# Kernel optimization log

Hardware: AMD Instinct MI355X
Metric: run time of the kernel (lower is better)

## Reference

```python
import jax, jax.numpy as jnp
import numpy as np

N_NODES = 10000
N_EDGES = 640000
IN_DIM = 128
NUM_HEADS = 8
OUT_DIM = 16  # per-head dim; NUM_HEADS*OUT_DIM == IN_DIM


def setup_inputs() -> dict:
    key = jax.random.key(0)
    ks = jax.random.split(key, 12)
    h = jax.random.normal(ks[0], (N_NODES, IN_DIM), dtype=jnp.float32)
    e = jax.random.normal(ks[1], (N_EDGES, IN_DIM), dtype=jnp.float32)
    src = jax.random.randint(ks[2], (N_EDGES,), 0, N_NODES, dtype=jnp.int32)
    dst = jax.random.randint(ks[3], (N_EDGES,), 0, N_NODES, dtype=jnp.int32)
    HD = NUM_HEADS * OUT_DIM
    scale = 0.05
    Wq = jax.random.normal(ks[4], (HD, IN_DIM), dtype=jnp.float32) * scale
    bq = jax.random.normal(ks[5], (HD,), dtype=jnp.float32) * scale
    Wk = jax.random.normal(ks[6], (HD, IN_DIM), dtype=jnp.float32) * scale
    bk = jax.random.normal(ks[7], (HD,), dtype=jnp.float32) * scale
    We = jax.random.normal(ks[8], (HD, IN_DIM), dtype=jnp.float32) * scale
    be = jax.random.normal(ks[9], (HD,), dtype=jnp.float32) * scale
    Wv = jax.random.normal(ks[10], (HD, IN_DIM), dtype=jnp.float32) * scale
    bv = jax.random.normal(ks[11], (HD,), dtype=jnp.float32) * scale
    return {"h": h, "e": e, "src": src, "dst": dst,
            "Wq": Wq, "bq": bq, "Wk": Wk, "bk": bk,
            "We": We, "be": be, "Wv": Wv, "bv": bv}


def reference(h, e, src, dst, Wq, bq, Wk, bk, We, be, Wv, bv):
    N = h.shape[0]
    H, D = NUM_HEADS, OUT_DIM
    # Linear projections (torch Linear: x @ W.T + b), reshape to [*, H, D]
    Q_h = (h @ Wq.T + bq).reshape(N, H, D)
    K_h = (h @ Wk.T + bk).reshape(N, H, D)
    V_h = (h @ Wv.T + bv).reshape(N, H, D)
    E_e = (e @ We.T + be).reshape(-1, H, D)
    # per-edge score: (K[src] * Q[dst]) / sqrt(D) * E  -> exp(clamp(sum(-1)))
    score = K_h[src] * Q_h[dst] / jnp.sqrt(jnp.float32(D)) * E_e  # [E, H, D]
    score_soft = jnp.exp(jnp.clip(score.sum(-1, keepdims=True), -5.0, 5.0))  # [E, H, 1]
    # scatter-sum aggregation to destination nodes
    wV = jax.ops.segment_sum(V_h[src] * score_soft, dst, num_segments=N)  # [N, H, D]
    z = jax.ops.segment_sum(score_soft, dst, num_segments=N)  # [N, H, 1]
    h_out = wV / (z + 1e-6)
    # dropout p=0.0 (eval): identity
    return h_out
```

## Files before the change

### kernel.cpp

```cpp
#include <hip/hip_runtime.h>
#include <hip/hip_bf16.h>

#define N_NODES 10000
#define N_EDGES 640000
#define HD 128
#define NH 8
#define TPAD 136

typedef __attribute__((ext_vector_type(4))) float floatx4;
typedef __attribute__((ext_vector_type(8))) __bf16 bf16x8;

__device__ __forceinline__ float b2f(unsigned short u) {
    union { unsigned int i; float f; } x;
    x.i = ((unsigned int)u) << 16;
    return x.f;
}
__device__ __forceinline__ unsigned short f2b(float f) {
    union { float f; unsigned int i; } x; x.f = f;
    unsigned int r = x.i + 0x7FFF + ((x.i >> 16) & 1);
    return (unsigned short)(r >> 16);
}

template<bool F32>
__device__ __forceinline__ float ld1(const void* p, size_t i) {
    if (F32) return ((const float*)p)[i];
    return b2f(((const unsigned short*)p)[i]);
}
template<bool F32>
__device__ __forceinline__ void ld8(const void* p, size_t i, float* out) {
    if (F32) {
        floatx4 a = *(const floatx4*)((const float*)p + i);
        floatx4 b = *(const floatx4*)((const float*)p + i + 4);
        out[0]=a[0]; out[1]=a[1]; out[2]=a[2]; out[3]=a[3];
        out[4]=b[0]; out[5]=b[1]; out[6]=b[2]; out[7]=b[3];
    } else {
        uint4 u = *(const uint4*)((const unsigned short*)p + i);
        const unsigned short* s = (const unsigned short*)&u;
        #pragma unroll
        for (int j = 0; j < 8; ++j) out[j] = b2f(s[j]);
    }
}
template<bool F32>
__device__ __forceinline__ uint4 ld8b(const void* p, size_t i) {
    if (F32) {
        float f[8]; ld8<true>(p, i, f);
        union { unsigned short s[8]; uint4 u; } r;
        #pragma unroll
        for (int j = 0; j < 8; ++j) r.s[j] = f2b(f[j]);
        return r.u;
    }
    return *(const uint4*)((const unsigned short*)p + i);
}

__global__ void k_sniff(const unsigned short* __restrict__ h,
                        int* __restrict__ wcnt, int* __restrict__ flag) {
    int t = threadIdx.x;
    int w = 0;
    #pragma unroll
    for (int j = 0; j < 16; ++j) {
        unsigned short u = h[t * 16 + j];
        int ex = (u >> 7) & 0xFF;
        if (ex >= 0x8F) ++w;
    }
    atomicAdd(wcnt, w);
    __threadfence();
    __syncthreads();
    if (t == 0) {
        int c = atomicAdd(wcnt, 0);
        *flag = (c > 64) ? 1 : 0;
    }
}

template<bool F32>
__device__ __forceinline__ void qkv_body(
    float (*hs)[HD],
    const void* __restrict__ h,
    const void* __restrict__ Wq, const void* __restrict__ bq,
    const void* __restrict__ Wk, const void* __restrict__ bk,
    const void* __restrict__ Wv, const void* __restrict__ bv,
    float* __restrict__ Qs, float* __restrict__ Kg, float* __restrict__ Vg)
{
    const int n0 = blockIdx.x * 8;
    const int d = threadIdx.x;
    #pragma unroll
    for (int r = 0; r < 8; ++r)
        hs[r][d] = ld1<F32>(h, (size_t)(n0 + r) * HD + d);
    __syncthreads();

    float aq[8], ak[8], av[8];
    #pragma unroll
    for (int i = 0; i < 8; ++i) { aq[i] = 0.f; ak[i] = 0.f; av[i] = 0.f; }

    for (int c = 0; c < 16; ++c) {
        float wqf[8], wkf[8], wvf[8];
        ld8<F32>(Wq, (size_t)d * HD + c * 8, wqf);
        ld8<F32>(Wk, (size_t)d * HD + c * 8, wkf);
        ld8<F32>(Wv, (size_t)d * HD + c * 8, wvf);
        #pragma unroll
        for (int n = 0; n < 8; ++n) {
            #pragma unroll
            for (int j = 0; j < 8; ++j) {
                float hv = hs[n][c * 8 + j];
                aq[n] += wqf[j] * hv;
                ak[n] += wkf[j] * hv;
                av[n] += wvf[j] * hv;
            }
        }
    }
    const float bqd = ld1<F32>(bq, d), bkd = ld1<F32>(bk, d), bvd = ld1<F32>(bv, d);
    #pragma unroll
    for (int n = 0; n < 8; ++n) {
        size_t o = (size_t)(n0 + n) * HD + d;
        Qs[o] = 0.25f * (aq[n] + bqd);
        Kg[o] = ak[n] + bkd;
        Vg[o] = av[n] + bvd;
    }
}

__global__ __launch_bounds__(128) void k_qkv(
    const void* h, const void* Wq, const void* bq, const void* Wk, const void* bk,
    const void* Wv, const void* bv,
    float* Qs, float* Kg, float* Vg, const int* flag)
{
    __shared__ float hs[8][HD];
    if (*flag) qkv_body<true >(hs, h, Wq, bq, Wk, bk, Wv, bv, Qs, Kg, Vg);
    else       qkv_body<false>(hs, h, Wq, bq, Wk, bk, Wv, bv, Qs, Kg, Vg);
}

__global__ void k_hist(const int* __restrict__ dst, int* __restrict__ cnt) {
    int i = blockIdx.x * blockDim.x + threadIdx.x;
    if (i < N_EDGES) {
        int d = dst[i];
        d = max(0, min(d, N_NODES - 1));
        atomicAdd(&cnt[d], 1);
    }
}

__global__ __launch_bounds__(1024) void k_scan(const int* __restrict__ cnt,
                                               int* __restrict__ cursor) {
    __shared__ int tmp[1024];
    const int tid = threadIdx.x;
    int carry = 0;
    for (int base = 0; base < N_NODES; base += 1024) {
        int i = base + tid;
        int v = (i < N_NODES) ? cnt[i] : 0;
        tmp[tid] = v;
        __syncthreads();
        for (int off = 1; off < 1024; off <<= 1) {
            int t = (tid >= off) ? tmp[tid - off] : 0;
            __syncthreads();
            tmp[tid] += t;
            __syncthreads();
        }
        if (i < N_NODES) cursor[i] = carry + tmp[tid] - v;
        int tot = tmp[1023];
        __syncthreads();
        carry += tot;
    }
}

__global__ void k_place(const int* __restrict__ dst, int* __restrict__ cursor,
                        int* __restrict__ eorder) {
    int i = blockIdx.x * blockDim.x + threadIdx.x;
    if (i < N_EDGES) {
        int d = dst[i];
        d = max(0, min(d, N_NODES - 1));
        int pos = atomicAdd(&cursor[d], 1);
        pos = max(0, min(pos, N_EDGES - 1));
        eorder[pos] = i;
    }
}

struct EdgeSmem {
    unsigned short Ae[64][TPAD];
    unsigned short Wl[HD][TPAD];
    float bel[HD];
    float sc[64][NH];
    int eids[64], srcs[64], dsts[64];
};

template<bool F32>
__device__ __forceinline__ void edge_body(
    EdgeSmem& sm,
    const void* __restrict__ e,
    const void* __restrict__ We, const void* __restrict__ be,
    const int* __restrict__ src, const int* __restrict__ dst,
    const int* __restrict__ eorder,
    const float* __restrict__ Qs, const float* __restrict__ Kg,
    const float* __restrict__ Vg,
    float* __restrict__ wV, float* __restrict__ zacc)
{
    const int tid = threadIdx.x;
    const int tile = blockIdx.x;

    if (tid < 64) {
        int eid = eorder[tile * 64 + tid];
        eid = max(0, min(eid, N_EDGES - 1));
        sm.eids[tid] = eid;
        int s = src[eid]; s = max(0, min(s, N_NODES - 1));
        int d = dst[eid]; d = max(0, min(d, N_NODES - 1));
        sm.srcs[tid] = s;
        sm.dsts[tid] = d;
    }
    if (tid < HD) sm.bel[tid] = ld1<F32>(be, tid);
    {
        int row = tid >> 1, halfsel = tid & 1;
        uint4* lp = (uint4*)&sm.Wl[row][halfsel * 64];
        #pragma unroll
        for (int q = 0; q < 8; ++q)
            lp[q] = ld8b<F32>(We, (size_t)row * HD + halfsel * 64 + q * 8);
    }
    __syncthreads();
    {
        int row = tid >> 2, qq = tid & 3;
        size_t base = (size_t)sm.eids[row] * HD + qq * 32;
        uint4* lp = (uint4*)&sm.Ae[row][qq * 32];
        #pragma unroll
        for (int q = 0; q < 4; ++q)
            lp[q] = ld8b<F32>(e, base + q * 8);
    }
    __syncthreads();

    const int lane = tid & 63;
    const int w = tid >> 6;
    const int m0 = w * 16;
    const int col = lane & 15;
    const int lq = lane >> 4;

    for (int hh = 0; hh < NH; ++hh) {
        floatx4 acc = {0.f, 0.f, 0.f, 0.f};
        #pragma unroll
        for (int kt = 0; kt < 4; ++kt) {
            bf16x8 a = *(const bf16x8*)&sm.Ae[m0 + col][kt * 32 + lq * 8];
            bf16x8 b = *(const bf16x8*)&sm.Wl[hh * 16 + col][kt * 32 + lq * 8];
            acc = __builtin_amdgcn_mfma_f32_16x16x32_bf16(a, b, acc, 0, 0, 0);
        }
        float bev = sm.bel[hh * 16 + col];
        #pragma unroll
        for (int r = 0; r < 4; ++r) {
            int row = lq * 4 + r;
            int edge = m0 + row;
            int s_n = sm.srcs[edge], d_n = sm.dsts[edge];
            float kq = Kg[(size_t)s_n * HD + hh * 16 + col] *
                       Qs[(size_t)d_n * HD + hh * 16 + col];
            float p = (acc[r] + bev) * kq;
            p += __shfl_xor(p, 1);
            p += __shfl_xor(p, 2);
            p += __shfl_xor(p, 4);
            p += __shfl_xor(p, 8);
            if (col == 0) {
                p = fminf(fmaxf(p, -5.f), 5.f);
                sm.sc[edge][hh] = __expf(p);
            }
        }
    }
    __syncthreads();

    const int halfsel = tid >> 7;
    const int hd = tid & 127;
    const int hhead = hd >> 4;
    const int e0 = halfsel * 32;

    float vv[32];
    #pragma unroll
    for (int i = 0; i < 32; ++i)
        vv[i] = Vg[(size_t)sm.srcs[e0 + i] * HD + hd];

    float accv = 0.f, accz = 0.f;
    int cur = sm.dsts[e0];
    #pragma unroll
    for (int i = 0; i < 32; ++i) {
        int ed = e0 + i;
        int dn = sm.dsts[ed];
        if (dn != cur) {
            atomicAdd(&wV[(size_t)cur * HD + hd], accv);
            if ((hd & 15) == 0) atomicAdd(&zacc[cur * NH + hhead], accz);
            accv = 0.f; accz = 0.f; cur = dn;
        }
        float s = sm.sc[ed][hhead];
        accv += s * vv[i];
        accz += s;
    }
    atomicAdd(&wV[(size_t)cur * HD + hd], accv);
    if ((hd & 15) == 0) atomicAdd(&zacc[cur * NH + hhead], accz);
}

__global__ __launch_bounds__(256) void k_edge(
    const void* e, const void* We, const void* be,
    const int* src, const int* dst, const int* eorder,
    const float* Qs, const float* Kg, const float* Vg,
    float* wV, float* zacc, const int* flag)
{
    __shared__ EdgeSmem sm;
    if (*flag) edge_body<true >(sm, e, We, be, src, dst, eorder, Qs, Kg, Vg, wV, zacc);
    else       edge_body<false>(sm, e, We, be, src, dst, eorder, Qs, Kg, Vg, wV, zacc);
}

__global__ void k_final(const float* __restrict__ wV, const float* __restrict__ zacc,
                        void* __restrict__ out, const int* __restrict__ flag) {
    int i = blockIdx.x * blockDim.x + threadIdx.x;
    if (i < N_NODES * HD) {
        int node = i >> 7;
        int hh = (i & 127) >> 4;
        float v = wV[i] / (zacc[node * NH + hh] + 1e-6f);
        if (*flag) ((float*)out)[i] = v;
        else       ((unsigned short*)out)[i] = f2b(v);
    }
}

extern "C" void kernel_launch(void* const* d_in, const int* in_sizes, int n_in,
                              void* d_out, int out_size, void* d_ws, size_t ws_size,
                              hipStream_t stream) {
    const void* h  = d_in[0];
    const void* e  = d_in[1];
    const int* src = (const int*)d_in[2];
    const int* dst = (const int*)d_in[3];
    const void* Wq = d_in[4];
    const void* bq = d_in[5];
    const void* Wk = d_in[6];
    const void* bk = d_in[7];
    const void* We = d_in[8];
    const void* be = d_in[9];
    const void* Wv = d_in[10];
    const void* bv = d_in[11];

    char* ws = (char*)d_ws;
    float* Qs    = (float*)(ws + 0);
    float* Kg    = (float*)(ws + 5120000);
    float* Vg    = (float*)(ws + 10240000);
    int* eorder  = (int*)  (ws + 15360000);
    int* cursor  = (int*)  (ws + 17920000);
    float* wV    = (float*)(ws + 17960000);
    float* zacc  = (float*)(ws + 23080000);
    int* cnt     = (int*)  (ws + 23400000);
    int* flag    = (int*)  (ws + 23440000);
    int* wcnt    = (int*)  (ws + 23440004);

    hipMemsetAsync(ws + 17960000, 0, 5480008, stream);

    k_sniff<<<1, 256, 0, stream>>>((const unsigned short*)h, wcnt, flag);
    k_qkv<<<N_NODES / 8, 128, 0, stream>>>(h, Wq, bq, Wk, bk, Wv, bv, Qs, Kg, Vg, flag);
    k_hist<<<(N_EDGES + 255) / 256, 256, 0, stream>>>(dst, cnt);
    k_scan<<<1, 1024, 0, stream>>>(cnt, cursor);
    k_place<<<(N_EDGES + 255) / 256, 256, 0, stream>>>(dst, cursor, eorder);
    k_edge<<<N_EDGES / 64, 256, 0, stream>>>(e, We, be, src, dst, eorder,
                                             Qs, Kg, Vg, wV, zacc, flag);
    k_final<<<(N_NODES * HD + 255) / 256, 256, 0, stream>>>(wV, zacc, d_out, flag);
}
```

Before: 1.018 ms.

## Pre-transpose QKV weights, shuffle-based scan, keep We fragments in registers

A small new kernel transposes Wq/Wk/Wv so the QKV projection reads weights coalesced, and k_qkv now runs 256 threads with 4 nodes per half-block. The single-block scan replaces its shared-memory Hillis-Steele loop with wave shuffles plus a per-wave sum pass, cutting the number of barriers. The edge kernel drops the shared We tile: each wave keeps fragments for two heads in registers and loops over four edge groups, and launch bounds request 4 blocks per CU. The transposed weights reuse the eorder workspace region before eorder is written, and the larger register footprint may limit occupancy.

```diff
diff --git a/kernel.cpp b/kernel.cpp
--- a/kernel.cpp
+++ b/kernel.cpp
@@ -72,59 +72,86 @@
 }
 
 template<bool F32>
+__device__ __forceinline__ void wt_body(float (*tile)[33], const void* W,
+                                        float* __restrict__ WT) {
+    const int t  = blockIdx.x & 15;
+    const int tr = t >> 2, tc = t & 3;
+    const int cx = threadIdx.x & 31, ry = threadIdx.x >> 5;
+    #pragma unroll
+    for (int q = 0; q < 4; ++q) {
+        int row = tr * 32 + ry + q * 8;
+        tile[ry + q * 8][cx] = ld1<F32>(W, (size_t)row * HD + tc * 32 + cx);
+    }
+    __syncthreads();
+    #pragma unroll
+    for (int q = 0; q < 4; ++q) {
+        int orow = tc * 32 + ry + q * 8;
+        WT[(size_t)orow * HD + tr * 32 + cx] = tile[cx][ry + q * 8];
+    }
+}
+__global__ __launch_bounds__(256) void k_wt(
+    const void* Wq, const void* Wk, const void* Wv,
+    float* WTq, float* WTk, float* WTv, const int* flag) {
+    __shared__ float tile[32][33];
+    int m = blockIdx.x >> 4;
+    const void* W = (m == 0) ? Wq : (m == 1) ? Wk : Wv;
+    float* WT     = (m == 0) ? WTq : (m == 1) ? WTk : WTv;
+    if (*flag) wt_body<true >(tile, W, WT);
+    else       wt_body<false>(tile, W, WT);
+}
+
+template<bool F32>
 __device__ __forceinline__ void qkv_body(
     float (*hs)[HD],
     const void* __restrict__ h,
-    const void* __restrict__ Wq, const void* __restrict__ bq,
-    const void* __restrict__ Wk, const void* __restrict__ bk,
-    const void* __restrict__ Wv, const void* __restrict__ bv,
+    const float* __restrict__ WTq, const void* __restrict__ bq,
+    const float* __restrict__ WTk, const void* __restrict__ bk,
+    const float* __restrict__ WTv, const void* __restrict__ bv,
     float* __restrict__ Qs, float* __restrict__ Kg, float* __restrict__ Vg)
 {
     const int n0 = blockIdx.x * 8;
-    const int d = threadIdx.x;
-    #pragma unroll
-    for (int r = 0; r < 8; ++r)
-        hs[r][d] = ld1<F32>(h, (size_t)(n0 + r) * HD + d);
-    __syncthreads();
-
-    float aq[8], ak[8], av[8];
-    #pragma unroll
-    for (int i = 0; i < 8; ++i) { aq[i] = 0.f; ak[i] = 0.f; av[i] = 0.f; }
-
-    for (int c = 0; c < 16; ++c) {
-        float wqf[8], wkf[8], wvf[8];
-        ld8<F32>(Wq, (size_t)d * HD + c * 8, wqf);
-        ld8<F32>(Wk, (size_t)d * HD + c * 8, wkf);
-        ld8<F32>(Wv, (size_t)d * HD + c * 8, wvf);
-        #pragma unroll
-        for (int n = 0; n < 8; ++n) {
-            #pragma unroll
-            for (int j = 0; j < 8; ++j) {
-                float hv = hs[n][c * 8 + j];
-                aq[n] += wqf[j] * hv;
-                ak[n] += wkf[j] * hv;
-                av[n] += wvf[j] * hv;
-            }
+    const int d = threadIdx.x & 127;
+    const int g = threadIdx.x >> 7;
+    #pragma unroll
+    for (int r = 0; r < 4; ++r)
+        hs[g * 4 + r][d] = ld1<F32>(h, (size_t)(n0 + g * 4 + r) * HD + d);
+    __syncthreads();
+
+    float aq[4], ak[4], av[4];
+    #pragma unroll
+    for (int i = 0; i < 4; ++i) { aq[i] = 0.f; ak[i] = 0.f; av[i] = 0.f; }
+
+    #pragma unroll 4
+    for (int c = 0; c < HD; ++c) {
+        float wq = WTq[c * HD + d];
+        float wk = WTk[c * HD + d];
+        float wv = WTv[c * HD + d];
+        #pragma unroll
+        for (int n = 0; n < 4; ++n) {
+            float hv = hs[g * 4 + n][c];
+            aq[n] += wq * hv;
+            ak[n] += wk * hv;
+            av[n] += wv * hv;
         }
     }
     const float bqd = ld1<F32>(bq, d), bkd = ld1<F32>(bk, d), bvd = ld1<F32>(bv, d);
     #pragma unroll
-    for (int n = 0; n < 8; ++n) {
-        size_t o = (size_t)(n0 + n) * HD + d;
+    for (int n = 0; n < 4; ++n) {
+        size_t o = (size_t)(n0 + g * 4 + n) * HD + d;
         Qs[o] = 0.25f * (aq[n] + bqd);
         Kg[o] = ak[n] + bkd;
         Vg[o] = av[n] + bvd;
     }
 }
 
-__global__ __launch_bounds__(128) void k_qkv(
-    const void* h, const void* Wq, const void* bq, const void* Wk, const void* bk,
-    const void* Wv, const void* bv,
+__global__ __launch_bounds__(256) void k_qkv(
+    const void* h, const float* WTq, const void* bq, const float* WTk,
+    const void* bk, const float* WTv, const void* bv,
     float* Qs, float* Kg, float* Vg, const int* flag)
 {
     __shared__ float hs[8][HD];
-    if (*flag) qkv_body<true >(hs, h, Wq, bq, Wk, bk, Wv, bv, Qs, Kg, Vg);
-    else       qkv_body<false>(hs, h, Wq, bq, Wk, bk, Wv, bv, Qs, Kg, Vg);
+    if (*flag) qkv_body<true >(hs, h, WTq, bq, WTk, bk, WTv, bv, Qs, Kg, Vg);
+    else       qkv_body<false>(hs, h, WTq, bq, WTk, bk, WTv, bv, Qs, Kg, Vg);
 }
 
 __global__ void k_hist(const int* __restrict__ dst, int* __restrict__ cnt) {
@@ -138,24 +165,35 @@
 
 __global__ __launch_bounds__(1024) void k_scan(const int* __restrict__ cnt,
                                                int* __restrict__ cursor) {
-    __shared__ int tmp[1024];
+    __shared__ int wsum[16];
     const int tid = threadIdx.x;
+    const int lane = tid & 63, wv = tid >> 6;
     int carry = 0;
     for (int base = 0; base < N_NODES; base += 1024) {
         int i = base + tid;
         int v = (i < N_NODES) ? cnt[i] : 0;
-        tmp[tid] = v;
+        int s = v;
+        #pragma unroll
+        for (int off = 1; off < 64; off <<= 1) {
+            int t = __shfl_up(s, off);
+            if (lane >= off) s += t;
+        }
+        if (lane == 63) wsum[wv] = s;
         __syncthreads();
-        for (int off = 1; off < 1024; off <<= 1) {
-            int t = (tid >= off) ? tmp[tid - off] : 0;
-            __syncthreads();
-            tmp[tid] += t;
-            __syncthreads();
-        }
-        if (i < N_NODES) cursor[i] = carry + tmp[tid] - v;
-        int tot = tmp[1023];
+        if (wv == 0) {
+            int wsv = (lane < 16) ? wsum[lane] : 0;
+            #pragma unroll
+            for (int off = 1; off < 16; off <<= 1) {
+                int t = __shfl_up(wsv, off);
+                if (lane >= off) wsv += t;
+            }
+            if (lane < 16) wsum[lane] = wsv;
+        }
         __syncthreads();
-        carry += tot;
+        int wbase = (wv == 0) ? 0 : wsum[wv - 1];
+        if (i < N_NODES) cursor[i] = carry + wbase + s - v;
+        carry += wsum[15];
+        __syncthreads();
     }
 }
 
@@ -173,8 +211,6 @@
 
 struct EdgeSmem {
     unsigned short Ae[64][TPAD];
-    unsigned short Wl[HD][TPAD];
-    float bel[HD];
     float sc[64][NH];
     int eids[64], srcs[64], dsts[64];
 };
@@ -192,23 +228,28 @@
 {
     const int tid = threadIdx.x;
     const int tile = blockIdx.x;
+    const int lane = tid & 63;
+    const int w = tid >> 6;
+    const int col = lane & 15;
+    const int lq = lane >> 4;
 
     if (tid < 64) {
         int eid = eorder[tile * 64 + tid];
         eid = max(0, min(eid, N_EDGES - 1));
         sm.eids[tid] = eid;
-        int s = src[eid]; s = max(0, min(s, N_NODES - 1));
-        int d = dst[eid]; d = max(0, min(d, N_NODES - 1));
-        sm.srcs[tid] = s;
-        sm.dsts[tid] = d;
-    }
-    if (tid < HD) sm.bel[tid] = ld1<F32>(be, tid);
-    {
-        int row = tid >> 1, halfsel = tid & 1;
-        uint4* lp = (uint4*)&sm.Wl[row][halfsel * 64];
-        #pragma unroll
-        for (int q = 0; q < 8; ++q)
-            lp[q] = ld8b<F32>(We, (size_t)row * HD + halfsel * 64 + q * 8);
+        int s = src[eid]; sm.srcs[tid] = max(0, min(s, N_NODES - 1));
+        int d = dst[eid]; sm.dsts[tid] = max(0, min(d, N_NODES - 1));
+    }
+
+    uint4 wfr[2][4];
+    float bev[2];
+    #pragma unroll
+    for (int hp = 0; hp < 2; ++hp) {
+        int row = (w * 2 + hp) * 16 + col;
+        bev[hp] = ld1<F32>(be, row);
+        #pragma unroll
+        for (int kt = 0; kt < 4; ++kt)
+            wfr[hp][kt] = ld8b<F32>(We, (size_t)row * HD + kt * 32 + lq * 8);
     }
     __syncthreads();
     {
@@ -221,36 +262,33 @@
     }
     __syncthreads();
 
-    const int lane = tid & 63;
-    const int w = tid >> 6;
-    const int m0 = w * 16;
-    const int col = lane & 15;
-    const int lq = lane >> 4;
-
-    for (int hh = 0; hh < NH; ++hh) {
-        floatx4 acc = {0.f, 0.f, 0.f, 0.f};
-        #pragma unroll
-        for (int kt = 0; kt < 4; ++kt) {
-            bf16x8 a = *(const bf16x8*)&sm.Ae[m0 + col][kt * 32 + lq * 8];
-            bf16x8 b = *(const bf16x8*)&sm.Wl[hh * 16 + col][kt * 32 + lq * 8];
-            acc = __builtin_amdgcn_mfma_f32_16x16x32_bf16(a, b, acc, 0, 0, 0);
-        }
-        float bev = sm.bel[hh * 16 + col];
-        #pragma unroll
-        for (int r = 0; r < 4; ++r) {
-            int row = lq * 4 + r;
-            int edge = m0 + row;
-            int s_n = sm.srcs[edge], d_n = sm.dsts[edge];
-            float kq = Kg[(size_t)s_n * HD + hh * 16 + col] *
-                       Qs[(size_t)d_n * HD + hh * 16 + col];
-            float p = (acc[r] + bev) * kq;
-            p += __shfl_xor(p, 1);
-            p += __shfl_xor(p, 2);
-            p += __shfl_xor(p, 4);
-            p += __shfl_xor(p, 8);
-            if (col == 0) {
-                p = fminf(fmaxf(p, -5.f), 5.f);
-                sm.sc[edge][hh] = __expf(p);
+    #pragma unroll
+    for (int hp = 0; hp < 2; ++hp) {
+        const int hh = w * 2 + hp;
+        #pragma unroll
+        for (int g = 0; g < 4; ++g) {
+            floatx4 acc = {0.f, 0.f, 0.f, 0.f};
+            #pragma unroll
+            for (int kt = 0; kt < 4; ++kt) {
+                bf16x8 a = *(const bf16x8*)&sm.Ae[g * 16 + col][kt * 32 + lq * 8];
+                bf16x8 b = *(const bf16x8*)&wfr[hp][kt];
+                acc = __builtin_amdgcn_mfma_f32_16x16x32_bf16(a, b, acc, 0, 0, 0);
+            }
+            #pragma unroll
+            for (int r = 0; r < 4; ++r) {
+                int edge = g * 16 + lq * 4 + r;
+                int s_n = sm.srcs[edge], d_n = sm.dsts[edge];
+                float kq = Kg[(size_t)s_n * HD + hh * 16 + col] *
+                           Qs[(size_t)d_n * HD + hh * 16 + col];
+                float p = (acc[r] + bev[hp]) * kq;
+                p += __shfl_xor(p, 1);
+                p += __shfl_xor(p, 2);
+                p += __shfl_xor(p, 4);
+                p += __shfl_xor(p, 8);
+                if (col == 0) {
+                    p = fminf(fmaxf(p, -5.f), 5.f);
+                    sm.sc[edge][hh] = __expf(p);
+                }
             }
         }
     }
@@ -285,7 +323,7 @@
     if ((hd & 15) == 0) atomicAdd(&zacc[cur * NH + hhead], accz);
 }
 
-__global__ __launch_bounds__(256) void k_edge(
+__global__ __launch_bounds__(256, 4) void k_edge(
     const void* e, const void* We, const void* be,
     const int* src, const int* dst, const int* eorder,
     const float* Qs, const float* Kg, const float* Vg,
@@ -335,11 +373,16 @@
     int* cnt     = (int*)  (ws + 23400000);
     int* flag    = (int*)  (ws + 23440000);
     int* wcnt    = (int*)  (ws + 23440004);
+    float* WTq   = (float*)(ws + 15360000);
+    float* WTk   = (float*)(ws + 15425536);
+    float* WTv   = (float*)(ws + 15491072);
 
     hipMemsetAsync(ws + 17960000, 0, 5480008, stream);
 
     k_sniff<<<1, 256, 0, stream>>>((const unsigned short*)h, wcnt, flag);
-    k_qkv<<<N_NODES / 8, 128, 0, stream>>>(h, Wq, bq, Wk, bk, Wv, bv, Qs, Kg, Vg, flag);
+    k_wt<<<48, 256, 0, stream>>>(Wq, Wk, Wv, WTq, WTk, WTv, flag);
+    k_qkv<<<N_NODES / 8, 256, 0, stream>>>(h, WTq, bq, WTk, bk, WTv, bv,
+                                           Qs, Kg, Vg, flag);
     k_hist<<<(N_EDGES + 255) / 256, 256, 0, stream>>>(dst, cnt);
     k_scan<<<1, 1024, 0, stream>>>(cnt, cursor);
     k_place<<<(N_EDGES + 255) / 256, 256, 0, stream>>>(dst, cursor, eorder);
```

Result: faster. 977.9 us (-3.9%).
